# Kernel optimization log

Measured on AMD Instinct MI355X. Metric: run time of the kernel, lower is better.

## Reference

```python
import jax, jax.numpy as jnp
import numpy as np

B, T, D = 4096, 200, 64
H1, H2 = 80, 40
C = 64  # cate_count


def setup_inputs() -> dict:
    key = jax.random.key(0)
    ks = jax.random.split(key, 12)
    q = jax.random.normal(ks[0], (B, D), dtype=jnp.float32)
    k = jax.random.normal(ks[1], (B, T, D), dtype=jnp.float32)
    mask = jax.random.randint(ks[2], (B, T), 0, 2, dtype=jnp.int32)
    hist_cate = jax.random.randint(ks[3], (B, T), 0, C, dtype=jnp.int32)
    # attention MLP params (Dense(80, PReLU), Dense(40, PReLU), Dense(1))
    W1 = jax.random.normal(ks[4], (4 * D, H1), dtype=jnp.float32) * (1.0 / np.sqrt(4 * D))
    b1 = jnp.zeros((H1,), dtype=jnp.float32)
    a1 = jnp.full((H1,), 0.25, dtype=jnp.float32)  # PReLU slopes
    W2 = jax.random.normal(ks[5], (H1, H2), dtype=jnp.float32) * (1.0 / np.sqrt(H1))
    b2 = jnp.zeros((H2,), dtype=jnp.float32)
    a2 = jnp.full((H2,), 0.25, dtype=jnp.float32)
    Wf = jax.random.normal(ks[6], (H2, 1), dtype=jnp.float32) * (1.0 / np.sqrt(H2))
    bf = jnp.zeros((1,), dtype=jnp.float32)
    return {
        "q": q, "k": k, "mask": mask, "hist_cate": hist_cate,
        "cate_count": C,
        "W1": W1, "b1": b1, "a1": a1,
        "W2": W2, "b2": b2, "a2": a2,
        "Wf": Wf, "bf": bf,
    }


def _prelu(x, alpha):
    return jnp.maximum(x, 0.0) + alpha * jnp.minimum(x, 0.0)


def reference(q, k, mask, hist_cate, cate_count, W1, b1, a1, W2, b2, a2, Wf, bf):
    b, t, d = k.shape
    qe = jnp.broadcast_to(q[:, None, :], (b, t, d))          # tile q over seq
    info = jnp.concatenate([qe, k, qe - k, qe * k], axis=-1)  # [B,T,4D]
    h = _prelu(info @ W1 + b1, a1)                            # [B,T,H1]
    h = _prelu(h @ W2 + b2, a2)                               # [B,T,H2]
    logits = (h @ Wf + bf)[..., 0]                            # [B,T]
    neg = jnp.float32(-2 ** 32 + 1)
    logits = jnp.where(mask == 0, neg, logits)
    logits = logits / jnp.sqrt(jnp.float32(d))
    w = jax.nn.softmax(logits, axis=-1)                       # [B,T]
    user_interest = jnp.einsum('bt,btd->bd', w, k)            # [B,D]
    # fused per-category masked weighted pooling (replaces Python loop)
    onehot = (hist_cate[:, None, :] == jnp.arange(cate_count, dtype=hist_cate.dtype)[None, :, None])  # [B,C,T]
    wc = w[:, None, :] * onehot.astype(w.dtype)               # [B,C,T]
    wc = wc / (jnp.sum(wc, axis=-1, keepdims=True) + 1e-10)
    cate_hidden = jnp.einsum('bct,btd->bcd', wc, k)           # [B,C,D]
    return user_interest, cate_hidden
```

## Files before the change

### kernel.cpp

```cpp
#include <hip/hip_runtime.h>

typedef unsigned short u16;
typedef short short8 __attribute__((ext_vector_type(8)));
typedef float f32x4 __attribute__((ext_vector_type(4)));

#define NEG_MASK -4294967295.0f

__device__ __forceinline__ u16 f2bf(float f) {
    unsigned int x = __float_as_uint(f);
    unsigned int r = (x + 0x7FFFu + ((x >> 16) & 1u)) >> 16;
    return (u16)r;
}
__device__ __forceinline__ short8 cvt8(float4 a, float4 b) {
    union { short8 v; u16 u[8]; } r;
    r.u[0] = f2bf(a.x); r.u[1] = f2bf(a.y); r.u[2] = f2bf(a.z); r.u[3] = f2bf(a.w);
    r.u[4] = f2bf(b.x); r.u[5] = f2bf(b.y); r.u[6] = f2bf(b.z); r.u[7] = f2bf(b.w);
    return r.v;
}

__global__ __launch_bounds__(256) void din_kernel(
    const float* __restrict__ qp, const float* __restrict__ kp,
    const int* __restrict__ maskp, const int* __restrict__ catep,
    const float* __restrict__ W1p, const float* __restrict__ b1p,
    const float* __restrict__ a1p, const float* __restrict__ W2p,
    const float* __restrict__ b2p, const float* __restrict__ a2p,
    const float* __restrict__ wfp, const float* __restrict__ bfp,
    float* __restrict__ outp)
{
    __shared__ __align__(16) u16 MtW2t[80*72 + 48*104];
    __shared__ __align__(16) u16 H1p[4*16*104];
    __shared__ float logits_s[200];
    __shared__ float q_s[64], qW_s[80], a1_s[80];
    __shared__ float a2_s[48], b2_s[48], wf_s[48];
    __shared__ float s_c[64], red_s[8], bf_s;
    __shared__ int cate_s[200];

    u16* Mt  = MtW2t;
    u16* W2t = MtW2t + 80*72;
    float* cate_acc = (float*)MtW2t;
    float* qW2 = logits_s;

    const int tid  = threadIdx.x;
    const int b    = blockIdx.x;
    const int wid  = tid >> 6;
    const int lane = tid & 63;
    const int i16  = lane & 15;
    const int q4   = lane >> 4;
    const float* kb = kp + (size_t)b * 12800;

    {
        unsigned int* w2z = (unsigned int*)W2t;
        for (int i = tid; i < (48*104)/2; i += 256) w2z[i] = 0u;
    }
    for (int i = tid; i < 4*16*12; i += 256) {
        int buf = i / 192, rem = i % 192, row = rem / 12, j = rem % 12;
        *(unsigned int*)&H1p[buf*(16*104) + row*104 + 80 + j*2] = 0u;
    }
    if (tid < 64) { s_c[tid] = 0.f; q_s[tid] = qp[(size_t)b*64 + tid]; }
    if (tid < 48) {
        wf_s[tid] = (tid < 40) ? wfp[tid] : 0.f;
        a2_s[tid] = (tid < 40) ? a2p[tid] : 0.f;
        b2_s[tid] = (tid < 40) ? b2p[tid] : 0.f;
    }
    if (tid < 80) a1_s[tid] = a1p[tid];
    if (tid == 0) bf_s = bfp[0];
    if (tid < 200) cate_s[tid] = catep[(size_t)b*200 + tid];
    __syncthreads();

    for (int j = tid; j < 5120; j += 256) {
        int d = j / 80, h = j - d*80;
        float m = W1p[5120 + j] - W1p[10240 + j] + q_s[d] * W1p[15360 + j];
        Mt[h*72 + d] = f2bf(m);
    }
    if (tid < 160) {
        int p = tid >> 7 ? 1 : (tid / 80), h = tid - (tid / 80) * 80;
        p = tid / 80;
        float acc = 0.f;
        int d0 = p * 32;
        #pragma unroll 4
        for (int d = d0; d < d0 + 32; ++d)
            acc += q_s[d] * (W1p[d*80 + h] + W1p[(128+d)*80 + h]);
        qW2[tid] = acc;
    }
    for (int e = tid; e < 3200; e += 256) {
        int n = e % 40, kk = e / 40;
        W2t[n*104 + kk] = f2bf(W2p[e]);
    }
    __syncthreads();
    if (tid < 80) qW_s[tid] = b1p[tid] + qW2[tid] + qW2[80 + tid];
    __syncthreads();

    u16* hb = &H1p[wid * (16*104)];
    for (int mt = wid; mt < 13; mt += 4) {
        int arow = mt*16 + i16; if (arow > 199) arow = 199;
        const float4* kr = (const float4*)(kb + arow*64);
        float4 f0 = kr[2*q4], f1 = kr[2*q4 + 1];
        float4 f2 = kr[8 + 2*q4], f3 = kr[9 + 2*q4];
        short8 ka0 = cvt8(f0, f1);
        short8 ka1 = cvt8(f2, f3);
        #pragma unroll
        for (int nt = 0; nt < 5; ++nt) {
            int n0 = nt*16;
            float qwv = qW_s[n0 + i16];
            f32x4 acc = { qwv, qwv, qwv, qwv };
            short8 b0 = *(const short8*)&Mt[(n0+i16)*72 + q4*8];
            short8 b1 = *(const short8*)&Mt[(n0+i16)*72 + 32 + q4*8];
            acc = __builtin_amdgcn_mfma_f32_16x16x32_bf16(ka0, b0, acc, 0, 0, 0);
            acc = __builtin_amdgcn_mfma_f32_16x16x32_bf16(ka1, b1, acc, 0, 0, 0);
            float al = a1_s[n0 + i16];
            #pragma unroll
            for (int r = 0; r < 4; ++r) {
                float x = acc[r];
                float y = (x > 0.f) ? x : al * x;
                hb[(q4*4 + r)*104 + n0 + i16] = f2bf(y);
            }
        }
        short8 A0 = *(const short8*)&hb[i16*104 + q4*8];
        short8 A1 = *(const short8*)&hb[i16*104 + 32 + q4*8];
        short8 A2 = *(const short8*)&hb[i16*104 + 64 + q4*8];
        float part0 = 0.f, part1 = 0.f, part2 = 0.f, part3 = 0.f;
        #pragma unroll
        for (int nt = 0; nt < 3; ++nt) {
            int n0 = nt*16;
            float b2v = b2_s[n0 + i16];
            f32x4 acc = { b2v, b2v, b2v, b2v };
            short8 w0 = *(const short8*)&W2t[(n0+i16)*104 + q4*8];
            short8 w1 = *(const short8*)&W2t[(n0+i16)*104 + 32 + q4*8];
            short8 w2 = *(const short8*)&W2t[(n0+i16)*104 + 64 + q4*8];
            acc = __builtin_amdgcn_mfma_f32_16x16x32_bf16(A0, w0, acc, 0, 0, 0);
            acc = __builtin_amdgcn_mfma_f32_16x16x32_bf16(A1, w1, acc, 0, 0, 0);
            acc = __builtin_amdgcn_mfma_f32_16x16x32_bf16(A2, w2, acc, 0, 0, 0);
            float al2 = a2_s[n0 + i16];
            float wfv = wf_s[n0 + i16];
            float x, y;
            x = acc[0]; y = (x > 0.f) ? x : al2*x; part0 += y*wfv;
            x = acc[1]; y = (x > 0.f) ? x : al2*x; part1 += y*wfv;
            x = acc[2]; y = (x > 0.f) ? x : al2*x; part2 += y*wfv;
            x = acc[3]; y = (x > 0.f) ? x : al2*x; part3 += y*wfv;
        }
        #pragma unroll
        for (int off = 1; off < 16; off <<= 1) {
            part0 += __shfl_xor(part0, off, 64);
            part1 += __shfl_xor(part1, off, 64);
            part2 += __shfl_xor(part2, off, 64);
            part3 += __shfl_xor(part3, off, 64);
        }
        if (i16 == 0) {
            float p0[4] = { part0, part1, part2, part3 };
            #pragma unroll
            for (int r = 0; r < 4; ++r) {
                int t = mt*16 + q4*4 + r;
                if (t < 200) {
                    int mv = maskp[(size_t)b*200 + t];
                    float v = (mv == 0) ? NEG_MASK : (bf_s + p0[r]);
                    logits_s[t] = v * 0.125f;
                }
            }
        }
    }
    __syncthreads();

    for (int i = tid; i < 4096; i += 256) cate_acc[i] = 0.f;
    float x = (tid < 200) ? logits_s[tid] : -3.0e38f;
    float m = x;
    #pragma unroll
    for (int off = 32; off >= 1; off >>= 1) m = fmaxf(m, __shfl_xor(m, off, 64));
    if (lane == 0) red_s[wid] = m;
    __syncthreads();
    float mx = fmaxf(fmaxf(red_s[0], red_s[1]), fmaxf(red_s[2], red_s[3]));
    float e = (tid < 200) ? __expf(x - mx) : 0.f;
    float s = e;
    #pragma unroll
    for (int off = 32; off >= 1; off >>= 1) s += __shfl_xor(s, off, 64);
    if (lane == 0) red_s[4 + wid] = s;
    __syncthreads();
    float tot = red_s[4] + red_s[5] + red_s[6] + red_s[7];
    float wv = e / tot;
    if (tid < 200) {
        logits_s[tid] = wv;
        if (wv > 0.f) atomicAdd(&s_c[cate_s[tid]], wv);
    }
    __syncthreads();

    #pragma unroll 2
    for (int t = wid; t < 200; t += 4) {
        float wt = logits_s[t];
        if (wt > 0.f) {
            int c = cate_s[t];
            float kd = kb[t*64 + lane];
            atomicAdd(&cate_acc[c*64 + lane], wt * kd);
        }
    }
    __syncthreads();
    if (tid < 64) {
        float ui = 0.f;
        #pragma unroll 8
        for (int c = 0; c < 64; ++c) ui += cate_acc[c*64 + tid];
        outp[(size_t)b*64 + tid] = ui;
    }
    for (int i = tid; i < 4096; i += 256) {
        int c = i >> 6;
        float v = cate_acc[i] / (s_c[c] + 1e-10f);
        outp[(size_t)(4096*64) + (size_t)b*4096 + i] = v;
    }
}

extern "C" void kernel_launch(void* const* d_in, const int* in_sizes, int n_in,
                              void* d_out, int out_size, void* d_ws, size_t ws_size,
                              hipStream_t stream) {
    din_kernel<<<4096, 256, 0, stream>>>(
        (const float*)d_in[0],
        (const float*)d_in[1],
        (const int*)d_in[2],
        (const int*)d_in[3],
        (const float*)d_in[5],
        (const float*)d_in[6],
        (const float*)d_in[7],
        (const float*)d_in[8],
        (const float*)d_in[9],
        (const float*)d_in[10],
        (const float*)d_in[11],
        (const float*)d_in[12],
        (float*)d_out);
}
```

Before: 580.7 us.

## Prefetch k tiles in MLP loop, stage mask, batch k loads and vectorize stores

```diff
diff --git a/kernel.cpp b/kernel.cpp
--- a/kernel.cpp
+++ b/kernel.cpp
@@ -18,7 +18,7 @@
     return r.v;
 }
 
-__global__ __launch_bounds__(256) void din_kernel(
+__global__ __launch_bounds__(256, 4) void din_kernel(
     const float* __restrict__ qp, const float* __restrict__ kp,
     const int* __restrict__ maskp, const int* __restrict__ catep,
     const float* __restrict__ W1p, const float* __restrict__ b1p,
@@ -34,6 +34,7 @@
     __shared__ float a2_s[48], b2_s[48], wf_s[48];
     __shared__ float s_c[64], red_s[8], bf_s;
     __shared__ int cate_s[200];
+    __shared__ int mask_s[200];
 
     u16* Mt  = MtW2t;
     u16* W2t = MtW2t + 80*72;
@@ -64,24 +65,30 @@
     }
     if (tid < 80) a1_s[tid] = a1p[tid];
     if (tid == 0) bf_s = bfp[0];
-    if (tid < 200) cate_s[tid] = catep[(size_t)b*200 + tid];
-    __syncthreads();
-
+    if (tid < 200) {
+        cate_s[tid] = catep[(size_t)b*200 + tid];
+        mask_s[tid] = maskp[(size_t)b*200 + tid];
+    }
+    __syncthreads();
+
+    #pragma unroll 4
     for (int j = tid; j < 5120; j += 256) {
         int d = j / 80, h = j - d*80;
         float m = W1p[5120 + j] - W1p[10240 + j] + q_s[d] * W1p[15360 + j];
         Mt[h*72 + d] = f2bf(m);
     }
     if (tid < 160) {
-        int p = tid >> 7 ? 1 : (tid / 80), h = tid - (tid / 80) * 80;
-        p = tid / 80;
-        float acc = 0.f;
+        int p = tid / 80, h = tid - p*80;
+        float acc0 = 0.f, acc1 = 0.f;
         int d0 = p * 32;
         #pragma unroll 4
-        for (int d = d0; d < d0 + 32; ++d)
-            acc += q_s[d] * (W1p[d*80 + h] + W1p[(128+d)*80 + h]);
-        qW2[tid] = acc;
-    }
+        for (int d = d0; d < d0 + 32; d += 2) {
+            acc0 += q_s[d]   * (W1p[d*80 + h]     + W1p[(128+d)*80 + h]);
+            acc1 += q_s[d+1] * (W1p[(d+1)*80 + h] + W1p[(129+d)*80 + h]);
+        }
+        qW2[tid] = acc0 + acc1;
+    }
+    #pragma unroll 4
     for (int e = tid; e < 3200; e += 256) {
         int n = e % 40, kk = e / 40;
         W2t[n*104 + kk] = f2bf(W2p[e]);
@@ -91,76 +98,98 @@
     __syncthreads();
 
     u16* hb = &H1p[wid * (16*104)];
-    for (int mt = wid; mt < 13; mt += 4) {
-        int arow = mt*16 + i16; if (arow > 199) arow = 199;
-        const float4* kr = (const float4*)(kb + arow*64);
-        float4 f0 = kr[2*q4], f1 = kr[2*q4 + 1];
-        float4 f2 = kr[8 + 2*q4], f3 = kr[9 + 2*q4];
-        short8 ka0 = cvt8(f0, f1);
-        short8 ka1 = cvt8(f2, f3);
-        #pragma unroll
-        for (int nt = 0; nt < 5; ++nt) {
-            int n0 = nt*16;
-            float qwv = qW_s[n0 + i16];
-            f32x4 acc = { qwv, qwv, qwv, qwv };
-            short8 b0 = *(const short8*)&Mt[(n0+i16)*72 + q4*8];
-            short8 b1 = *(const short8*)&Mt[(n0+i16)*72 + 32 + q4*8];
-            acc = __builtin_amdgcn_mfma_f32_16x16x32_bf16(ka0, b0, acc, 0, 0, 0);
-            acc = __builtin_amdgcn_mfma_f32_16x16x32_bf16(ka1, b1, acc, 0, 0, 0);
-            float al = a1_s[n0 + i16];
-            #pragma unroll
-            for (int r = 0; r < 4; ++r) {
-                float x = acc[r];
-                float y = (x > 0.f) ? x : al * x;
-                hb[(q4*4 + r)*104 + n0 + i16] = f2bf(y);
-            }
-        }
-        short8 A0 = *(const short8*)&hb[i16*104 + q4*8];
-        short8 A1 = *(const short8*)&hb[i16*104 + 32 + q4*8];
-        short8 A2 = *(const short8*)&hb[i16*104 + 64 + q4*8];
-        float part0 = 0.f, part1 = 0.f, part2 = 0.f, part3 = 0.f;
-        #pragma unroll
-        for (int nt = 0; nt < 3; ++nt) {
-            int n0 = nt*16;
-            float b2v = b2_s[n0 + i16];
-            f32x4 acc = { b2v, b2v, b2v, b2v };
-            short8 w0 = *(const short8*)&W2t[(n0+i16)*104 + q4*8];
-            short8 w1 = *(const short8*)&W2t[(n0+i16)*104 + 32 + q4*8];
-            short8 w2 = *(const short8*)&W2t[(n0+i16)*104 + 64 + q4*8];
-            acc = __builtin_amdgcn_mfma_f32_16x16x32_bf16(A0, w0, acc, 0, 0, 0);
-            acc = __builtin_amdgcn_mfma_f32_16x16x32_bf16(A1, w1, acc, 0, 0, 0);
-            acc = __builtin_amdgcn_mfma_f32_16x16x32_bf16(A2, w2, acc, 0, 0, 0);
-            float al2 = a2_s[n0 + i16];
-            float wfv = wf_s[n0 + i16];
-            float x, y;
-            x = acc[0]; y = (x > 0.f) ? x : al2*x; part0 += y*wfv;
-            x = acc[1]; y = (x > 0.f) ? x : al2*x; part1 += y*wfv;
-            x = acc[2]; y = (x > 0.f) ? x : al2*x; part2 += y*wfv;
-            x = acc[3]; y = (x > 0.f) ? x : al2*x; part3 += y*wfv;
-        }
-        #pragma unroll
-        for (int off = 1; off < 16; off <<= 1) {
-            part0 += __shfl_xor(part0, off, 64);
-            part1 += __shfl_xor(part1, off, 64);
-            part2 += __shfl_xor(part2, off, 64);
-            part3 += __shfl_xor(part3, off, 64);
-        }
-        if (i16 == 0) {
-            float p0[4] = { part0, part1, part2, part3 };
-            #pragma unroll
-            for (int r = 0; r < 4; ++r) {
-                int t = mt*16 + q4*4 + r;
-                if (t < 200) {
-                    int mv = maskp[(size_t)b*200 + t];
-                    float v = (mv == 0) ? NEG_MASK : (bf_s + p0[r]);
-                    logits_s[t] = v * 0.125f;
+    {
+        int mt = wid;
+        float4 f0, f1, f2, f3;
+        {
+            int arow = mt*16 + i16; if (arow > 199) arow = 199;
+            const float4* kr = (const float4*)(kb + arow*64);
+            f0 = kr[2*q4];     f1 = kr[2*q4 + 1];
+            f2 = kr[8 + 2*q4]; f3 = kr[9 + 2*q4];
+        }
+        for (; mt < 13; mt += 4) {
+            int nmt = mt + 4; if (nmt > 12) nmt = 12;
+            int narow = nmt*16 + i16; if (narow > 199) narow = 199;
+            const float4* nkr = (const float4*)(kb + narow*64);
+            float4 g0 = nkr[2*q4],     g1 = nkr[2*q4 + 1];
+            float4 g2 = nkr[8 + 2*q4], g3 = nkr[9 + 2*q4];
+
+            short8 ka0 = cvt8(f0, f1);
+            short8 ka1 = cvt8(f2, f3);
+            #pragma unroll
+            for (int nt = 0; nt < 5; ++nt) {
+                int n0 = nt*16;
+                float qwv = qW_s[n0 + i16];
+                f32x4 acc = { qwv, qwv, qwv, qwv };
+                short8 b0 = *(const short8*)&Mt[(n0+i16)*72 + q4*8];
+                short8 b1 = *(const short8*)&Mt[(n0+i16)*72 + 32 + q4*8];
+                acc = __builtin_amdgcn_mfma_f32_16x16x32_bf16(ka0, b0, acc, 0, 0, 0);
+                acc = __builtin_amdgcn_mfma_f32_16x16x32_bf16(ka1, b1, acc, 0, 0, 0);
+                float al = a1_s[n0 + i16];
+                #pragma unroll
+                for (int r = 0; r < 4; ++r) {
+                    float x = acc[r];
+                    float y = (x > 0.f) ? x : al * x;
+                    hb[(q4*4 + r)*104 + n0 + i16] = f2bf(y);
                 }
             }
-        }
-    }
-    __syncthreads();
-
-    for (int i = tid; i < 4096; i += 256) cate_acc[i] = 0.f;
+            short8 A0 = *(const short8*)&hb[i16*104 + q4*8];
+            short8 A1 = *(const short8*)&hb[i16*104 + 32 + q4*8];
+            short8 A2 = *(const short8*)&hb[i16*104 + 64 + q4*8];
+            float part0 = 0.f, part1 = 0.f, part2 = 0.f, part3 = 0.f;
+            #pragma unroll
+            for (int nt = 0; nt < 3; ++nt) {
+                int n0 = nt*16;
+                float b2v = b2_s[n0 + i16];
+                f32x4 acc = { b2v, b2v, b2v, b2v };
+                short8 w0 = *(const short8*)&W2t[(n0+i16)*104 + q4*8];
+                short8 w1 = *(const short8*)&W2t[(n0+i16)*104 + 32 + q4*8];
+                short8 w2 = *(const short8*)&W2t[(n0+i16)*104 + 64 + q4*8];
+                acc = __builtin_amdgcn_mfma_f32_16x16x32_bf16(A0, w0, acc, 0, 0, 0);
+                acc = __builtin_amdgcn_mfma_f32_16x16x32_bf16(A1, w1, acc, 0, 0, 0);
+                acc = __builtin_amdgcn_mfma_f32_16x16x32_bf16(A2, w2, acc, 0, 0, 0);
+                float al2 = a2_s[n0 + i16];
+                float wfv = wf_s[n0 + i16];
+                float x, y;
+                x = acc[0]; y = (x > 0.f) ? x : al2*x; part0 += y*wfv;
+                x = acc[1]; y = (x > 0.f) ? x : al2*x; part1 += y*wfv;
+                x = acc[2]; y = (x > 0.f) ? x : al2*x; part2 += y*wfv;
+                x = acc[3]; y = (x > 0.f) ? x : al2*x; part3 += y*wfv;
+            }
+            #pragma unroll
+            for (int off = 1; off < 16; off <<= 1) {
+                part0 += __shfl_xor(part0, off, 64);
+                part1 += __shfl_xor(part1, off, 64);
+                part2 += __shfl_xor(part2, off, 64);
+                part3 += __shfl_xor(part3, off, 64);
+            }
+            if (i16 == 0) {
+                float p0[4] = { part0, part1, part2, part3 };
+                #pragma unroll
+                for (int r = 0; r < 4; ++r) {
+                    int t = mt*16 + q4*4 + r;
+                    if (t < 200) {
+                        int mv = mask_s[t];
+                        float v = (mv == 0) ? NEG_MASK : (bf_s + p0[r]);
+                        logits_s[t] = v * 0.125f;
+                    }
+                }
+            }
+            f0 = g0; f1 = g1; f2 = g2; f3 = g3;
+        }
+    }
+    __syncthreads();
+
+    {
+        float4 z = {0.f, 0.f, 0.f, 0.f};
+        float4* ca4 = (float4*)cate_acc;
+        for (int i = tid; i < 1024; i += 256) ca4[i] = z;
+    }
+    const int t0 = wid * 50;
+    float kd[10];
+    #pragma unroll
+    for (int j = 0; j < 10; ++j) kd[j] = kb[(t0 + j)*64 + lane];
+
     float x = (tid < 200) ? logits_s[tid] : -3.0e38f;
     float m = x;
     #pragma unroll
@@ -182,26 +211,44 @@
     }
     __syncthreads();
 
-    #pragma unroll 2
-    for (int t = wid; t < 200; t += 4) {
-        float wt = logits_s[t];
-        if (wt > 0.f) {
-            int c = cate_s[t];
-            float kd = kb[t*64 + lane];
-            atomicAdd(&cate_acc[c*64 + lane], wt * kd);
-        }
-    }
-    __syncthreads();
+    for (int i = 0; i < 50; i += 10) {
+        float nkd[10];
+        const bool more = (i + 10 < 50);
+        if (more) {
+            #pragma unroll
+            for (int j = 0; j < 10; ++j) nkd[j] = kb[(t0 + i + 10 + j)*64 + lane];
+        }
+        float w_[10]; int c_[10];
+        #pragma unroll
+        for (int j = 0; j < 10; ++j) { w_[j] = logits_s[t0+i+j]; c_[j] = cate_s[t0+i+j]; }
+        #pragma unroll
+        for (int j = 0; j < 10; ++j) {
+            float w = w_[j];
+            if (w > 0.f) atomicAdd(&cate_acc[c_[j]*64 + lane], w * kd[j]);
+        }
+        if (more) {
+            #pragma unroll
+            for (int j = 0; j < 10; ++j) kd[j] = nkd[j];
+        }
+    }
+    __syncthreads();
+
     if (tid < 64) {
         float ui = 0.f;
         #pragma unroll 8
         for (int c = 0; c < 64; ++c) ui += cate_acc[c*64 + tid];
         outp[(size_t)b*64 + tid] = ui;
     }
-    for (int i = tid; i < 4096; i += 256) {
-        int c = i >> 6;
-        float v = cate_acc[i] / (s_c[c] + 1e-10f);
-        outp[(size_t)(4096*64) + (size_t)b*4096 + i] = v;
+    {
+        float* outc = outp + (size_t)(4096*64) + (size_t)b*4096;
+        #pragma unroll
+        for (int ii = 0; ii < 4; ++ii) {
+            int i = tid*4 + ii*1024;
+            float inv = 1.0f / (s_c[i >> 6] + 1e-10f);
+            float4 v = *(const float4*)&cate_acc[i];
+            v.x *= inv; v.y *= inv; v.z *= inv; v.w *= inv;
+            *(float4*)&outc[i] = v;
+        }
     }
 }
 
```

Measured after the change: 573.7 us. About the same (-1.2%).
